# Optimization experiments

Measured on AMD Instinct MI355X. Metric: run time of the kernel, lower is better.

The kernel has to match this reference:

```python
import jax, jax.numpy as jnp
import numpy as np

N_NODES = 50000
N_EDGES = 800000
N_GRAPHS = 512
F_IN = 128
D = 256
EPS = 1e-5
NEG_SLOPE = 0.01  # torch LeakyReLU default


def leaky_relu(x):
    return jnp.where(x >= 0, x, NEG_SLOPE * x)


def egnn_conv(x, edge_index, edge_attr, lin2_w, lin2_b, lin_w, lin_b, n_nodes):
    # message: LeakyReLU(lin(x_j + lin2(edge_attr))), aggregate: add at target i
    src, dst = edge_index[0], edge_index[1]
    ea = edge_attr @ lin2_w.T + lin2_b          # [E, in]
    msg = (x[src] + ea) @ lin_w.T + lin_b        # [E, out]
    msg = leaky_relu(msg)
    return jax.ops.segment_sum(msg, dst, num_segments=n_nodes)


def batch_norm(x, w, b):
    # training-mode BatchNorm1d: biased batch statistics over node axis
    mean = jnp.mean(x, axis=0)
    var = jnp.mean(jnp.square(x - mean), axis=0)
    return (x - mean) * jax.lax.rsqrt(var + EPS) * w + b


def setup_inputs() -> dict:
    key = jax.random.key(0)
    ks = jax.random.split(key, 8)
    inp = {
        "node_ids": jax.random.randint(ks[0], (N_NODES,), 0, 51),
        "edge_index": jax.random.randint(ks[1], (2, N_EDGES), 0, N_NODES),
        "edge_attr": jax.random.normal(ks[2], (N_EDGES, 4), dtype=jnp.float32),
        "batch": jnp.sort(jax.random.randint(ks[3], (N_NODES,), 0, N_GRAPHS)),
        "emb_table": jax.random.normal(ks[4], (51, F_IN), dtype=jnp.float32) * 0.1,
        "c1_lin2_w": jax.random.normal(ks[5], (F_IN, 4), dtype=jnp.float32) * 0.1,
        "c1_lin2_b": jnp.zeros((F_IN,), jnp.float32),
        "c1_lin_w": jax.random.normal(ks[6], (D, F_IN), dtype=jnp.float32) * (1.0 / np.sqrt(F_IN)),
        "c1_lin_b": jnp.zeros((D,), jnp.float32),
        "bn1_w": jnp.ones((D,), jnp.float32),
        "bn1_b": jnp.zeros((D,), jnp.float32),
        "c2_lin2_w": jax.random.normal(jax.random.fold_in(key, 10), (D, 4), dtype=jnp.float32) * 0.1,
        "c2_lin2_b": jnp.zeros((D,), jnp.float32),
        "c2_lin_w": jax.random.normal(ks[7], (D, D), dtype=jnp.float32) * (1.0 / np.sqrt(D)),
        "c2_lin_b": jnp.zeros((D,), jnp.float32),
        "bn2_w": jnp.ones((D,), jnp.float32),
        "bn2_b": jnp.zeros((D,), jnp.float32),
        "gate_w": jax.random.normal(jax.random.fold_in(key, 11), (1, D), dtype=jnp.float32) * 0.1,
        "gate_b": jnp.zeros((1,), jnp.float32),
    }
    return inp


def reference(node_ids, edge_index, edge_attr, batch, emb_table,
              c1_lin2_w, c1_lin2_b, c1_lin_w, c1_lin_b, bn1_w, bn1_b,
              c2_lin2_w, c2_lin2_b, c2_lin_w, c2_lin_b, bn2_w, bn2_b,
              gate_w, gate_b):
    x = emb_table[node_ids]                                   # [N, F_IN]
    x = egnn_conv(x, edge_index, edge_attr, c1_lin2_w, c1_lin2_b,
                  c1_lin_w, c1_lin_b, N_NODES)                # [N, D]
    x = leaky_relu(batch_norm(x, bn1_w, bn1_b))
    x2 = egnn_conv(x, edge_index, edge_attr, c2_lin2_w, c2_lin2_b,
                   c2_lin_w, c2_lin_b, N_NODES)               # [N, D]
    x2 = leaky_relu(batch_norm(x2, bn2_w, bn2_b))
    # AttentionalAggregation: softmax of gate over each graph segment
    gate = x2 @ gate_w.T + gate_b                             # [N, 1]
    gmax = jax.ops.segment_max(gate, batch, num_segments=N_GRAPHS)
    e = jnp.exp(gate - gmax[batch])                           # [N, 1]
    denom = jax.ops.segment_sum(e, batch, num_segments=N_GRAPHS)
    alpha = e / denom[batch]
    out = jax.ops.segment_sum(alpha * x2, batch, num_segments=N_GRAPHS)
    return out                                                # [G, D]
```

## Files before the change

### kernel.cpp

```cpp
#include <hip/hip_runtime.h>
#include <hip/hip_bf16.h>

#define NN 50000
#define NE 800000
#define NG 512

typedef __bf16 bf16_t;
typedef __bf16 bf16x8 __attribute__((ext_vector_type(8)));
typedef __bf16 bf16x4 __attribute__((ext_vector_type(4)));
typedef float f32x4 __attribute__((ext_vector_type(4)));
typedef float f32x2 __attribute__((ext_vector_type(2)));

__device__ __forceinline__ float lrelu(float v) { return v >= 0.f ? v : 0.01f * v; }

__device__ __forceinline__ f32x2 unpk2(unsigned w) {
    union { unsigned u; float f; } lo, hi;
    lo.u = w << 16;
    hi.u = w & 0xffff0000u;
    f32x2 r; r[0] = lo.f; r[1] = hi.f; return r;
}

__device__ __forceinline__ int vzero() {
    int vz;
    asm("v_mov_b32 %0, 0" : "=v"(vz));
    return vz;
}

__global__ void gme_setup(const float* __restrict__ emb,
                          const float* __restrict__ c1lw, const float* __restrict__ c1l2w,
                          const float* __restrict__ c1l2b, const float* __restrict__ c1lb,
                          const float* __restrict__ c2lw, const float* __restrict__ c2l2w,
                          const float* __restrict__ c2l2b, const float* __restrict__ c2lb,
                          bf16_t* __restrict__ TYB, float* __restrict__ WC1,
                          float* __restrict__ WC2, float* __restrict__ CB2,
                          bf16_t* __restrict__ W2B) {
    int b = blockIdx.x, t = threadIdx.x;
    if (b < 51) {
        const float4* er = (const float4*)(emb + b * 128);
        const float4* zb = (const float4*)c1l2b;
        const float4* wr = (const float4*)(c1lw + t * 128);
        float s = 0.f;
        for (int k = 0; k < 32; ++k) {
            float4 e = er[k], z = zb[k], w = wr[k];
            s += (e.x + z.x) * w.x + (e.y + z.y) * w.y + (e.z + z.z) * w.z + (e.w + z.w) * w.w;
        }
        TYB[b * 256 + t] = (bf16_t)(s + c1lb[t]);
    } else if (b == 51) {
        const float4* wr = (const float4*)(c1lw + t * 128);
        const float4* cw = (const float4*)c1l2w;
        float4 a = make_float4(0.f, 0.f, 0.f, 0.f);
        for (int k = 0; k < 32; ++k) {
            float4 w = wr[k];
            float4 c0 = cw[k * 4 + 0], c1 = cw[k * 4 + 1], c2 = cw[k * 4 + 2], c3 = cw[k * 4 + 3];
            a.x += w.x * c0.x + w.y * c1.x + w.z * c2.x + w.w * c3.x;
            a.y += w.x * c0.y + w.y * c1.y + w.z * c2.y + w.w * c3.y;
            a.z += w.x * c0.z + w.y * c1.z + w.z * c2.z + w.w * c3.z;
            a.w += w.x * c0.w + w.y * c1.w + w.z * c2.w + w.w * c3.w;
        }
        ((float4*)WC1)[t] = a;
    } else if (b == 52) {
        const float4* wr = (const float4*)(c2lw + t * 256);
        const float4* cw = (const float4*)c2l2w;
        const float4* zb = (const float4*)c2l2b;
        float4 a = make_float4(0.f, 0.f, 0.f, 0.f);
        float ab = 0.f;
        for (int k = 0; k < 64; ++k) {
            float4 w = wr[k];
            float4 c0 = cw[k * 4 + 0], c1 = cw[k * 4 + 1], c2 = cw[k * 4 + 2], c3 = cw[k * 4 + 3];
            float4 z = zb[k];
            a.x += w.x * c0.x + w.y * c1.x + w.z * c2.x + w.w * c3.x;
            a.y += w.x * c0.y + w.y * c1.y + w.z * c2.y + w.w * c3.y;
            a.z += w.x * c0.z + w.y * c1.z + w.z * c2.z + w.w * c3.z;
            a.w += w.x * c0.w + w.y * c1.w + w.z * c2.w + w.w * c3.w;
            ab += w.x * z.x + w.y * z.y + w.z * z.z + w.w * z.w;
        }
        ((float4*)WC2)[t] = a;
        CB2[t] = ab + c2lb[t];
    } else {
        int i0 = (b - 53) * 1024;
        for (int r = 0; r < 4; ++r) {
            int i = i0 + r * 256 + t;
            W2B[i] = (bf16_t)c2lw[i];
        }
    }
}

__global__ void gme_count(const int* __restrict__ ei, int* __restrict__ cnt) {
    int e = blockIdx.x * 256 + threadIdx.x;
    if (e >= NE) return;
    atomicAdd(&cnt[ei[NE + e]], 1);
}

__global__ void gme_scan1(const int* __restrict__ CNT, int* __restrict__ LP,
                          int* __restrict__ BS) {
    __shared__ int lds[256];
    int b = blockIdx.x, t = threadIdx.x;
    int i = b * 196 + t;
    int v = (t < 196 && i < NN) ? CNT[i] : 0;
    lds[t] = v;
    __syncthreads();
    for (int off = 1; off < 256; off <<= 1) {
        int u = (t >= off) ? lds[t - off] : 0;
        __syncthreads();
        lds[t] += u;
        __syncthreads();
    }
    if (t < 196 && i < NN) LP[i] = lds[t] - v;
    if (t == 255) BS[b] = lds[255];
}

__global__ void gme_scan2(const int* __restrict__ BS, int* __restrict__ BX,
                          int* __restrict__ RS) {
    __shared__ int lds[256];
    int t = threadIdx.x;
    int v = BS[t];
    lds[t] = v;
    __syncthreads();
    for (int off = 1; off < 256; off <<= 1) {
        int u = (t >= off) ? lds[t - off] : 0;
        __syncthreads();
        lds[t] += u;
        __syncthreads();
    }
    BX[t] = lds[t] - v;
    if (t == 255) RS[NN] = lds[255];
}

__global__ void gme_scan3(const int* __restrict__ LP, const int* __restrict__ BX,
                          int* __restrict__ RS, int* __restrict__ CUR) {
    int b = blockIdx.x, t = threadIdx.x;
    if (t >= 196) return;
    int i = b * 196 + t;
    if (i >= NN) return;
    int v = BX[b] + LP[i];
    RS[i] = v;
    CUR[i] = v;
}

__global__ void gme_scatter(const int* __restrict__ ei,
                            const float4* __restrict__ eattr,
                            const int* __restrict__ node_ids,
                            int* __restrict__ CUR, int* __restrict__ SM,
                            float4* __restrict__ SattrP) {
    int e = blockIdx.x * 256 + threadIdx.x;
    if (e >= NE) return;
    int s = ei[e];
    int d = ei[NE + e];
    int nid = node_ids[s];
    int pos = atomicAdd(&CUR[d], 1);
    SM[pos] = s | (nid << 16);
    SattrP[pos] = eattr[e];
}

__global__ __launch_bounds__(256) void gme_conv0(
        const int* __restrict__ RS, const int* __restrict__ SM,
        const float4* __restrict__ SattrP, const bf16_t* __restrict__ TYB,
        const float* __restrict__ Wc, float* __restrict__ agg) {
    __shared__ __align__(16) uint2 sTY[51 * 64];
    {
        const uint4* s4 = (const uint4*)TYB;
        uint4* d4 = (uint4*)sTY;
        for (int i = threadIdx.x; i < 51 * 32; i += 256) d4[i] = s4[i];
    }
    __syncthreads();
    int lane = threadIdx.x & 63;
    int vz = vzero();
    const float4* wc4 = (const float4*)Wc;
    int c4 = lane * 4;
    float4 w0 = wc4[c4 + 0], w1 = wc4[c4 + 1], w2 = wc4[c4 + 2], w3 = wc4[c4 + 3];
    f32x2 wA0 = {w0.x, w1.x}, wB0 = {w0.y, w1.y}, wC0 = {w0.z, w1.z}, wD0 = {w0.w, w1.w};
    f32x2 wA1 = {w2.x, w3.x}, wB1 = {w2.y, w3.y}, wC1 = {w2.z, w3.z}, wD1 = {w2.w, w3.w};
    const f32x2 zero = {0.f, 0.f};
    const uint2* lrow = sTY + lane;
    int base = blockIdx.x * 16 + (threadIdx.x >> 6) * 4;
#pragma unroll 1
    for (int k = 0; k < 4; ++k) {
        int node = __builtin_amdgcn_readfirstlane(base + k);
        int rs = RS[node], re = RS[node + 1];
        f32x2 accP0 = zero, accP1 = zero, accA0 = zero, accA1 = zero;
        auto accum = [&](float4 a, uint2 r) {
            f32x2 y0 = unpk2(r.x), y1 = unpk2(r.y);
            f32x2 ax = {a.x, a.x}, ay = {a.y, a.y}, az = {a.z, a.z}, aw = {a.w, a.w};
            f32x2 m0 = __builtin_elementwise_fma(ax, wA0, y0);
            f32x2 m1 = __builtin_elementwise_fma(ax, wA1, y1);
            m0 = __builtin_elementwise_fma(ay, wB0, m0);
            m1 = __builtin_elementwise_fma(ay, wB1, m1);
            m0 = __builtin_elementwise_fma(az, wC0, m0);
            m1 = __builtin_elementwise_fma(az, wC1, m1);
            m0 = __builtin_elementwise_fma(aw, wD0, m0);
            m1 = __builtin_elementwise_fma(aw, wD1, m1);
            accA0 += m0; accA1 += m1;
            accP0 += __builtin_elementwise_max(m0, zero);
            accP1 += __builtin_elementwise_max(m1, zero);
        };
        int j = rs;
        for (; j + 8 <= re; j += 8) {
            int m[8]; float4 a[8]; uint2 r[8];
#pragma unroll
            for (int u = 0; u < 8; ++u) m[u] = SM[j + u + vz];
#pragma unroll
            for (int u = 0; u < 8; ++u) a[u] = SattrP[j + u + vz];
#pragma unroll
            for (int u = 0; u < 8; ++u) r[u] = lrow[(m[u] >> 16) << 6];
#pragma unroll
            for (int u = 0; u < 8; ++u) accum(a[u], r[u]);
        }
        if (j + 4 <= re) {
            int m[4]; float4 a[4]; uint2 r[4];
#pragma unroll
            for (int u = 0; u < 4; ++u) m[u] = SM[j + u + vz];
#pragma unroll
            for (int u = 0; u < 4; ++u) a[u] = SattrP[j + u + vz];
#pragma unroll
            for (int u = 0; u < 4; ++u) r[u] = lrow[(m[u] >> 16) << 6];
#pragma unroll
            for (int u = 0; u < 4; ++u) accum(a[u], r[u]);
            j += 4;
        }
        for (; j < re; ++j) {
            int m = SM[j + vz];
            accum(SattrP[j + vz], lrow[(m >> 16) << 6]);
        }
        const f32x2 c99 = {0.99f, 0.99f}, c01 = {0.01f, 0.01f};
        f32x2 o0 = __builtin_elementwise_fma(accP0, c99, accA0 * c01);
        f32x2 o1 = __builtin_elementwise_fma(accP1, c99, accA1 * c01);
        *((float4*)(agg + node * 256) + lane) = make_float4(o0[0], o0[1], o1[0], o1[1]);
    }
}

__global__ __launch_bounds__(256, 4) void gme_conv1(
        const int* __restrict__ RS, const int* __restrict__ SM,
        const float4* __restrict__ SattrP, const bf16_t* __restrict__ QB,
        const float* __restrict__ Wc, float* __restrict__ agg) {
    int lane = threadIdx.x & 63;
    int node = __builtin_amdgcn_readfirstlane(blockIdx.x * 4 + (threadIdx.x >> 6));
    if (node >= NN) return;
    const float4* wc4 = (const float4*)Wc;
    int c4 = lane * 4;
    float4 w0 = wc4[c4 + 0], w1 = wc4[c4 + 1], w2 = wc4[c4 + 2], w3 = wc4[c4 + 3];
    f32x2 wA0 = {w0.x, w1.x}, wB0 = {w0.y, w1.y}, wC0 = {w0.z, w1.z}, wD0 = {w0.w, w1.w};
    f32x2 wA1 = {w2.x, w3.x}, wB1 = {w2.y, w3.y}, wC1 = {w2.z, w3.z}, wD1 = {w2.w, w3.w};
    const f32x2 zero = {0.f, 0.f};
    f32x2 accP0 = zero, accP1 = zero, accA0 = zero, accA1 = zero;
    int rs = RS[node], re = RS[node + 1];
    const char* yb = (const char*)QB;
    unsigned loff = (unsigned)(lane << 3);
    auto rowld = [&](int row) -> uint2 {
        return *(const uint2*)(yb + ((unsigned)row << 9) + loff);
    };
    auto accum = [&](float4 a, uint2 r) {
        f32x2 y0 = unpk2(r.x), y1 = unpk2(r.y);
        f32x2 ax = {a.x, a.x}, ay = {a.y, a.y}, az = {a.z, a.z}, aw = {a.w, a.w};
        f32x2 m0 = __builtin_elementwise_fma(ax, wA0, y0);
        f32x2 m1 = __builtin_elementwise_fma(ax, wA1, y1);
        m0 = __builtin_elementwise_fma(ay, wB0, m0);
        m1 = __builtin_elementwise_fma(ay, wB1, m1);
        m0 = __builtin_elementwise_fma(az, wC0, m0);
        m1 = __builtin_elementwise_fma(az, wC1, m1);
        m0 = __builtin_elementwise_fma(aw, wD0, m0);
        m1 = __builtin_elementwise_fma(aw, wD1, m1);
        accA0 += m0; accA1 += m1;
        accP0 += __builtin_elementwise_max(m0, zero);
        accP1 += __builtin_elementwise_max(m1, zero);
    };
    int j = rs;
    for (; j + 12 <= re; j += 12) {
        int s[12]; float4 a[12]; uint2 r[12];
#pragma unroll
        for (int u = 0; u < 12; ++u) s[u] = SM[j + u];
#pragma unroll
        for (int u = 0; u < 12; ++u) r[u] = rowld(s[u] & 0xffff);
#pragma unroll
        for (int u = 0; u < 12; ++u) a[u] = SattrP[j + u];
#pragma unroll
        for (int u = 0; u < 12; ++u) accum(a[u], r[u]);
    }
    if (j + 8 <= re) {
        int s[8]; float4 a[8]; uint2 r[8];
#pragma unroll
        for (int u = 0; u < 8; ++u) s[u] = SM[j + u];
#pragma unroll
        for (int u = 0; u < 8; ++u) r[u] = rowld(s[u] & 0xffff);
#pragma unroll
        for (int u = 0; u < 8; ++u) a[u] = SattrP[j + u];
#pragma unroll
        for (int u = 0; u < 8; ++u) accum(a[u], r[u]);
        j += 8;
    }
    if (j + 4 <= re) {
        int s[4]; float4 a[4]; uint2 r[4];
#pragma unroll
        for (int u = 0; u < 4; ++u) s[u] = SM[j + u];
#pragma unroll
        for (int u = 0; u < 4; ++u) r[u] = rowld(s[u] & 0xffff);
#pragma unroll
        for (int u = 0; u < 4; ++u) a[u] = SattrP[j + u];
#pragma unroll
        for (int u = 0; u < 4; ++u) accum(a[u], r[u]);
        j += 4;
    }
    for (; j < re; ++j) accum(SattrP[j], rowld(SM[j] & 0xffff));
    const f32x2 c99 = {0.99f, 0.99f}, c01 = {0.01f, 0.01f};
    f32x2 o0 = __builtin_elementwise_fma(accP0, c99, accA0 * c01);
    f32x2 o1 = __builtin_elementwise_fma(accP1, c99, accA1 * c01);
    *((float4*)(agg + node * 256) + lane) = make_float4(o0[0], o0[1], o1[0], o1[1]);
}

__global__ __launch_bounds__(256) void gme_bns1(const float* __restrict__ P,
                                                float* __restrict__ PART) {
    __shared__ float ls[4][256], lq[4][256];
    int lane = threadIdx.x & 63;
    int w = threadIdx.x >> 6;
    int b = blockIdx.x;
    int r0 = b * 98;
    int r1 = r0 + 98; if (r1 > NN) r1 = NN;
    float4 s = make_float4(0, 0, 0, 0), q = make_float4(0, 0, 0, 0);
    for (int n = r0 + w; n < r1; n += 4) {
        float4 v = ((const float4*)P)[n * 64 + lane];
        s.x += v.x; s.y += v.y; s.z += v.z; s.w += v.w;
        q.x += v.x * v.x; q.y += v.y * v.y; q.z += v.z * v.z; q.w += v.w * v.w;
    }
    int c = lane * 4;
    ls[w][c] = s.x; ls[w][c + 1] = s.y; ls[w][c + 2] = s.z; ls[w][c + 3] = s.w;
    lq[w][c] = q.x; lq[w][c + 1] = q.y; lq[w][c + 2] = q.z; lq[w][c + 3] = q.w;
    __syncthreads();
    if (w == 0) {
#pragma unroll
        for (int k = 0; k < 4; ++k) {
            int cc = c + k;
            PART[b * 512 + cc] = ls[0][cc] + ls[1][cc] + ls[2][cc] + ls[3][cc];
            PART[b * 512 + 256 + cc] = lq[0][cc] + lq[1][cc] + lq[2][cc] + lq[3][cc];
        }
    }
}

__global__ __launch_bounds__(512) void gme_bns2(const float* __restrict__ PART,
                                                float* __restrict__ ST) {
    int t = threadIdx.x;
    int b = blockIdx.x;
    float acc = 0.f;
#pragma unroll
    for (int r = 0; r < 32; ++r) acc += PART[(b * 32 + r) * 512 + t];
    atomicAdd(&ST[t], acc);
}

__global__ __launch_bounds__(256) void gme_gemm(const float* __restrict__ P,
                                                const float* __restrict__ ST,
                                                const float* __restrict__ bw,
                                                const float* __restrict__ bb,
                                                const bf16_t* __restrict__ W2B,
                                                const float* __restrict__ CB2,
                                                bf16_t* __restrict__ QB) {
    __shared__ float s_sc[256], s_sh[256];
    __shared__ __align__(16) uint4 sB[8192];
    {
        int c = threadIdx.x;
        float mean = ST[c] * (1.f / NN);
        float var = ST[256 + c] * (1.f / NN) - mean * mean;
        float sc = bw[c] * rsqrtf(var + 1e-5f);
        s_sc[c] = sc;
        s_sh[c] = bb[c] - mean * sc;
        const uint4* w4 = (const uint4*)W2B;
#pragma unroll
        for (int it = 0; it < 32; ++it) {
            int i = it * 256 + c;
            int row = i >> 5, slot = i & 31;
            sB[(row << 5) | (slot ^ (row & 7))] = w4[i];
        }
    }
    __syncthreads();
    int lane = threadIdx.x & 63;
    int wave = blockIdx.x * 4 + (threadIdx.x >> 6);
    if (wave >= NN / 16) return;
    int m0 = wave * 16;
    int r = lane & 15, q = lane >> 4;
    int rx = r & 7;
    const float* arow = P + (m0 + r) * 256 + q * 8;
    bf16x8 a[8];
#pragma unroll
    for (int kt = 0; kt < 8; ++kt) {
        int k0 = kt * 32 + q * 8;
        float4 u0 = *(const float4*)(arow + kt * 32);
        float4 u1 = *(const float4*)(arow + kt * 32 + 4);
        bf16x8 f;
        f[0] = (bf16_t)lrelu(fmaf(u0.x, s_sc[k0 + 0], s_sh[k0 + 0]));
        f[1] = (bf16_t)lrelu(fmaf(u0.y, s_sc[k0 + 1], s_sh[k0 + 1]));
        f[2] = (bf16_t)lrelu(fmaf(u0.z, s_sc[k0 + 2], s_sh[k0 + 2]));
        f[3] = (bf16_t)lrelu(fmaf(u0.w, s_sc[k0 + 3], s_sh[k0 + 3]));
        f[4] = (bf16_t)lrelu(fmaf(u1.x, s_sc[k0 + 4], s_sh[k0 + 4]));
        f[5] = (bf16_t)lrelu(fmaf(u1.y, s_sc[k0 + 5], s_sh[k0 + 5]));
        f[6] = (bf16_t)lrelu(fmaf(u1.z, s_sc[k0 + 6], s_sh[k0 + 6]));
        f[7] = (bf16_t)lrelu(fmaf(u1.w, s_sc[k0 + 7], s_sh[k0 + 7]));
        a[kt] = f;
    }
#pragma unroll 1
    for (int g = 0; g < 2; ++g) {
        f32x4 acc[8];
#pragma unroll
        for (int n8 = 0; n8 < 8; ++n8) acc[n8] = (f32x4){0.f, 0.f, 0.f, 0.f};
#pragma unroll
        for (int kt = 0; kt < 8; ++kt) {
            int slot = (kt * 4 + q) ^ rx;
            bf16x8 bf[8];
#pragma unroll
            for (int n8 = 0; n8 < 8; ++n8) {
                int row = g * 128 + n8 * 16 + r;
                bf[n8] = *(const bf16x8*)&sB[(row << 5) | slot];
            }
#pragma unroll
            for (int n8 = 0; n8 < 8; ++n8) {
                acc[n8] = __builtin_amdgcn_mfma_f32_16x16x32_bf16(bf[n8], a[kt], acc[n8], 0, 0, 0);
            }
        }
#pragma unroll
        for (int n8 = 0; n8 < 8; ++n8) {
            int nt = g * 8 + n8;
            float4 cbv = ((const float4*)CB2)[nt * 4 + q];
            bf16x4 o;
            o[0] = (bf16_t)(acc[n8][0] + cbv.x);
            o[1] = (bf16_t)(acc[n8][1] + cbv.y);
            o[2] = (bf16_t)(acc[n8][2] + cbv.z);
            o[3] = (bf16_t)(acc[n8][3] + cbv.w);
            *(bf16x4*)(QB + (m0 + r) * 256 + nt * 16 + q * 4) = o;
        }
    }
}

__global__ void gme_gstart(const int* __restrict__ batch, int* __restrict__ GS) {
    int n = blockIdx.x * 256 + threadIdx.x;
    if (n >= NN) return;
    int b = batch[n];
    if (n == 0) {
        for (int g = 0; g <= b; ++g) GS[g] = 0;
    } else {
        int a = batch[n - 1];
        for (int g = a + 1; g <= b; ++g) GS[g] = n;
    }
    if (n == NN - 1) {
        for (int g = b + 1; g <= NG; ++g) GS[g] = NN;
    }
}

__global__ __launch_bounds__(256) void gme_attn(const int* __restrict__ GS,
                                                const float* __restrict__ P,
                                                const float* __restrict__ ST,
                                                const float* __restrict__ bw,
                                                const float* __restrict__ bb,
                                                const float* __restrict__ gw,
                                                const float* __restrict__ gb,
                                                float* __restrict__ out) {
    __shared__ float gl[1024];
    __shared__ float rr[8];
    int g = blockIdx.x, t = threadIdx.x;
    int lo = GS[g], hi = GS[g + 1];
    if (lo >= hi) { out[g * 256 + t] = 0.f; return; }
    int lane = t & 63, w = t >> 6;
    {
        float4 s4 = ((const float4*)ST)[lane];
        float4 q4 = ((const float4*)(ST + 256))[lane];
        float4 w4 = ((const float4*)bw)[lane];
        float4 b4 = ((const float4*)bb)[lane];
        float4 g4 = ((const float4*)gw)[lane];
        float m0 = s4.x * (1.f / NN), m1 = s4.y * (1.f / NN);
        float m2 = s4.z * (1.f / NN), m3 = s4.w * (1.f / NN);
        float sc0 = w4.x * rsqrtf(q4.x * (1.f / NN) - m0 * m0 + 1e-5f);
        float sc1 = w4.y * rsqrtf(q4.y * (1.f / NN) - m1 * m1 + 1e-5f);
        float sc2 = w4.z * rsqrtf(q4.z * (1.f / NN) - m2 * m2 + 1e-5f);
        float sc3 = w4.w * rsqrtf(q4.w * (1.f / NN) - m3 * m3 + 1e-5f);
        float sh0 = b4.x - m0 * sc0, sh1 = b4.y - m1 * sc1;
        float sh2 = b4.z - m2 * sc2, sh3 = b4.w - m3 * sc3;
        float gb0 = gb[0];
        for (int n = lo + w; n < hi; n += 4) {
            float4 p = *(const float4*)(P + n * 256 + lane * 4);
            float d = lrelu(fmaf(p.x, sc0, sh0)) * g4.x
                    + lrelu(fmaf(p.y, sc1, sh1)) * g4.y
                    + lrelu(fmaf(p.z, sc2, sh2)) * g4.z
                    + lrelu(fmaf(p.w, sc3, sh3)) * g4.w;
#pragma unroll
            for (int off = 32; off > 0; off >>= 1) d += __shfl_xor(d, off, 64);
            if (lane == 0) gl[n - lo] = d + gb0;
        }
    }
    __syncthreads();
    int cnt = hi - lo;
    float lm = -3.0e38f;
    for (int i = t; i < cnt; i += 256) lm = fmaxf(lm, gl[i]);
#pragma unroll
    for (int off = 32; off > 0; off >>= 1) lm = fmaxf(lm, __shfl_xor(lm, off, 64));
    if (lane == 0) rr[w] = lm;
    __syncthreads();
    float mx = fmaxf(fmaxf(rr[0], rr[1]), fmaxf(rr[2], rr[3]));
    float ls = 0.f;
    for (int i = t; i < cnt; i += 256) { float e = expf(gl[i] - mx); gl[i] = e; ls += e; }
#pragma unroll
    for (int off = 32; off > 0; off >>= 1) ls += __shfl_xor(ls, off, 64);
    if (lane == 0) rr[4 + w] = ls;
    __syncthreads();
    float sinv = 1.f / (rr[4] + rr[5] + rr[6] + rr[7]);
    float mean = ST[t] * (1.f / NN);
    float var = ST[256 + t] * (1.f / NN) - mean * mean;
    float sc = bw[t] * rsqrtf(var + 1e-5f);
    float sh = bb[t] - mean * sc;
    float a0 = 0.f, a1 = 0.f, a2 = 0.f, a3 = 0.f;
    int n = lo;
    for (; n + 4 <= hi; n += 4) {
        float p0 = P[n * 256 + t], p1 = P[(n + 1) * 256 + t];
        float p2 = P[(n + 2) * 256 + t], p3 = P[(n + 3) * 256 + t];
        a0 = fmaf(gl[n - lo + 0], lrelu(fmaf(p0, sc, sh)), a0);
        a1 = fmaf(gl[n - lo + 1], lrelu(fmaf(p1, sc, sh)), a1);
        a2 = fmaf(gl[n - lo + 2], lrelu(fmaf(p2, sc, sh)), a2);
        a3 = fmaf(gl[n - lo + 3], lrelu(fmaf(p3, sc, sh)), a3);
    }
    for (; n < hi; ++n) a0 = fmaf(gl[n - lo], lrelu(fmaf(P[n * 256 + t], sc, sh)), a0);
    out[g * 256 + t] = (a0 + a1 + a2 + a3) * sinv;
}

extern "C" void kernel_launch(void* const* d_in, const int* in_sizes, int n_in,
                              void* d_out, int out_size, void* d_ws, size_t ws_size,
                              hipStream_t stream) {
    const int* node_ids = (const int*)d_in[0];
    const int* edge_index = (const int*)d_in[1];
    const float4* edge_attr = (const float4*)d_in[2];
    const int* batch = (const int*)d_in[3];
    const float* emb = (const float*)d_in[4];
    const float* c1l2w = (const float*)d_in[5];
    const float* c1l2b = (const float*)d_in[6];
    const float* c1lw = (const float*)d_in[7];
    const float* c1lb = (const float*)d_in[8];
    const float* bn1w = (const float*)d_in[9];
    const float* bn1b = (const float*)d_in[10];
    const float* c2l2w = (const float*)d_in[11];
    const float* c2l2b = (const float*)d_in[12];
    const float* c2lw = (const float*)d_in[13];
    const float* c2lb = (const float*)d_in[14];
    const float* bn2w = (const float*)d_in[15];
    const float* bn2b = (const float*)d_in[16];
    const float* gate_w = (const float*)d_in[17];
    const float* gate_b = (const float*)d_in[18];

    char* ws = (char*)d_ws;
    size_t oP = 0;
    size_t oQB = oP + 51200000;
    size_t oSattrP = oQB + 25600000;
    size_t oSM = oSattrP + 12800000;
    size_t oRS = oSM + 3200000;
    size_t oCNT = oRS + 200064;
    size_t oCUR = oCNT + 200000;
    size_t oLP = oCUR + 200000;
    size_t oBS = oLP + 200000;
    size_t oBX = oBS + 1024;
    size_t oTY = oBX + 1024;
    size_t oWC1 = oTY + 52224;
    size_t oWC2 = oWC1 + 4096;
    size_t oCB2 = oWC2 + 4096;
    size_t oW2B = oCB2 + 1024;
    size_t oST = oW2B + 131072;
    size_t oGS = oST + 4096;
    size_t oPART = oGS + 2064;

    float* P = (float*)(ws + oP);
    bf16_t* QB = (bf16_t*)(ws + oQB);
    float4* SattrP = (float4*)(ws + oSattrP);
    int* SM = (int*)(ws + oSM);
    int* RS = (int*)(ws + oRS);
    int* CNT = (int*)(ws + oCNT);
    int* CUR = (int*)(ws + oCUR);
    int* LP = (int*)(ws + oLP);
    int* BS = (int*)(ws + oBS);
    int* BX = (int*)(ws + oBX);
    bf16_t* TYB = (bf16_t*)(ws + oTY);
    float* WC1 = (float*)(ws + oWC1);
    float* WC2 = (float*)(ws + oWC2);
    float* CB2 = (float*)(ws + oCB2);
    bf16_t* W2B = (bf16_t*)(ws + oW2B);
    float* ST1 = (float*)(ws + oST);
    float* ST2 = ST1 + 512;
    int* GS = (int*)(ws + oGS);
    float* PART = (float*)(ws + oPART);

    hipMemsetAsync(CNT, 0, NN * sizeof(int), stream);
    hipMemsetAsync(ST1, 0, 4096, stream);

    gme_setup<<<117, 256, 0, stream>>>(emb, c1lw, c1l2w, c1l2b, c1lb,
                                       c2lw, c2l2w, c2l2b, c2lb,
                                       TYB, WC1, WC2, CB2, W2B);
    gme_count<<<NE / 256, 256, 0, stream>>>(edge_index, CNT);
    gme_scan1<<<256, 256, 0, stream>>>(CNT, LP, BS);
    gme_scan2<<<1, 256, 0, stream>>>(BS, BX, RS);
    gme_scan3<<<256, 256, 0, stream>>>(LP, BX, RS, CUR);
    gme_scatter<<<NE / 256, 256, 0, stream>>>(edge_index, edge_attr, node_ids,
                                              CUR, SM, SattrP);
    gme_gstart<<<(NN + 255) / 256, 256, 0, stream>>>(batch, GS);
    gme_conv0<<<NN / 16, 256, 0, stream>>>(RS, SM, SattrP, TYB, WC1, P);
    gme_bns1<<<512, 256, 0, stream>>>(P, PART);
    gme_bns2<<<16, 512, 0, stream>>>(PART, ST1);
    gme_gemm<<<(NN / 16 + 3) / 4, 256, 0, stream>>>(P, ST1, bn1w, bn1b, W2B, CB2, QB);
    gme_conv1<<<NN / 4, 256, 0, stream>>>(RS, SM, SattrP, QB, WC2, P);
    gme_bns1<<<512, 256, 0, stream>>>(P, PART);
    gme_bns2<<<16, 512, 0, stream>>>(PART, ST2);
    gme_attn<<<NG, 256, 0, stream>>>(GS, P, ST2, bn2w, bn2b, gate_w, gate_b,
                                     (float*)d_out);
}
```

Measured before the change: 409.6 us.

## Fuse first BatchNorm statistics into conv0 and deepen its edge-loop unroll

```diff
diff --git a/kernel.cpp b/kernel.cpp
--- a/kernel.cpp
+++ b/kernel.cpp
@@ -152,10 +152,11 @@
     SattrP[pos] = eattr[e];
 }
 
-__global__ __launch_bounds__(256) void gme_conv0(
+__global__ __launch_bounds__(256, 4) void gme_conv0(
         const int* __restrict__ RS, const int* __restrict__ SM,
         const float4* __restrict__ SattrP, const bf16_t* __restrict__ TYB,
-        const float* __restrict__ Wc, float* __restrict__ agg) {
+        const float* __restrict__ Wc, float* __restrict__ agg,
+        float* __restrict__ PART) {
     __shared__ __align__(16) uint2 sTY[51 * 64];
     {
         const uint4* s4 = (const uint4*)TYB;
@@ -164,6 +165,7 @@
     }
     __syncthreads();
     int lane = threadIdx.x & 63;
+    int w = threadIdx.x >> 6;
     int vz = vzero();
     const float4* wc4 = (const float4*)Wc;
     int c4 = lane * 4;
@@ -172,7 +174,8 @@
     f32x2 wA1 = {w2.x, w3.x}, wB1 = {w2.y, w3.y}, wC1 = {w2.z, w3.z}, wD1 = {w2.w, w3.w};
     const f32x2 zero = {0.f, 0.f};
     const uint2* lrow = sTY + lane;
-    int base = blockIdx.x * 16 + (threadIdx.x >> 6) * 4;
+    int base = blockIdx.x * 16 + w * 4;
+    f32x2 ssum0 = zero, ssum1 = zero, qsum0 = zero, qsum1 = zero;
 #pragma unroll 1
     for (int k = 0; k < 4; ++k) {
         int node = __builtin_amdgcn_readfirstlane(base + k);
@@ -194,25 +197,47 @@
             accP1 += __builtin_elementwise_max(m1, zero);
         };
         int j = rs;
-        for (; j + 8 <= re; j += 8) {
+        for (; j + 16 <= re; j += 16) {
+            int m[16]; uint2 r[16];
+#pragma unroll
+            for (int u = 0; u < 16; ++u) m[u] = SM[j + u + vz];
+#pragma unroll
+            for (int u = 0; u < 16; ++u) r[u] = lrow[(m[u] >> 16) << 6];
+            {
+                float4 a[8];
+#pragma unroll
+                for (int u = 0; u < 8; ++u) a[u] = SattrP[j + u + vz];
+#pragma unroll
+                for (int u = 0; u < 8; ++u) accum(a[u], r[u]);
+            }
+            {
+                float4 a[8];
+#pragma unroll
+                for (int u = 0; u < 8; ++u) a[u] = SattrP[j + 8 + u + vz];
+#pragma unroll
+                for (int u = 0; u < 8; ++u) accum(a[u], r[8 + u]);
+            }
+        }
+        if (j + 8 <= re) {
             int m[8]; float4 a[8]; uint2 r[8];
 #pragma unroll
             for (int u = 0; u < 8; ++u) m[u] = SM[j + u + vz];
 #pragma unroll
+            for (int u = 0; u < 8; ++u) r[u] = lrow[(m[u] >> 16) << 6];
+#pragma unroll
             for (int u = 0; u < 8; ++u) a[u] = SattrP[j + u + vz];
 #pragma unroll
-            for (int u = 0; u < 8; ++u) r[u] = lrow[(m[u] >> 16) << 6];
-#pragma unroll
             for (int u = 0; u < 8; ++u) accum(a[u], r[u]);
+            j += 8;
         }
         if (j + 4 <= re) {
             int m[4]; float4 a[4]; uint2 r[4];
 #pragma unroll
             for (int u = 0; u < 4; ++u) m[u] = SM[j + u + vz];
 #pragma unroll
+            for (int u = 0; u < 4; ++u) r[u] = lrow[(m[u] >> 16) << 6];
+#pragma unroll
             for (int u = 0; u < 4; ++u) a[u] = SattrP[j + u + vz];
-#pragma unroll
-            for (int u = 0; u < 4; ++u) r[u] = lrow[(m[u] >> 16) << 6];
 #pragma unroll
             for (int u = 0; u < 4; ++u) accum(a[u], r[u]);
             j += 4;
@@ -225,7 +250,21 @@
         f32x2 o0 = __builtin_elementwise_fma(accP0, c99, accA0 * c01);
         f32x2 o1 = __builtin_elementwise_fma(accP1, c99, accA1 * c01);
         *((float4*)(agg + node * 256) + lane) = make_float4(o0[0], o0[1], o1[0], o1[1]);
-    }
+        ssum0 += o0; ssum1 += o1;
+        qsum0 += o0 * o0; qsum1 += o1 * o1;
+    }
+    __syncthreads();
+    float* red = (float*)sTY;
+    red[w * 512 + c4 + 0] = ssum0[0]; red[w * 512 + c4 + 1] = ssum0[1];
+    red[w * 512 + c4 + 2] = ssum1[0]; red[w * 512 + c4 + 3] = ssum1[1];
+    red[w * 512 + 256 + c4 + 0] = qsum0[0]; red[w * 512 + 256 + c4 + 1] = qsum0[1];
+    red[w * 512 + 256 + c4 + 2] = qsum1[0]; red[w * 512 + 256 + c4 + 3] = qsum1[1];
+    __syncthreads();
+    int cc = threadIdx.x;
+    float s = red[cc] + red[512 + cc] + red[1024 + cc] + red[1536 + cc];
+    float q = red[256 + cc] + red[768 + cc] + red[1280 + cc] + red[1792 + cc];
+    PART[blockIdx.x * 512 + cc] = s;
+    PART[blockIdx.x * 512 + 256 + cc] = q;
 }
 
 __global__ __launch_bounds__(256, 4) void gme_conv1(
@@ -344,6 +383,17 @@
     atomicAdd(&ST[t], acc);
 }
 
+__global__ __launch_bounds__(512) void gme_bns2b(const float* __restrict__ PART,
+                                                 float* __restrict__ ST) {
+    int t = threadIdx.x;
+    int b = blockIdx.x;
+    int r0 = b * 32;
+    int r1 = r0 + 32; if (r1 > 3125) r1 = 3125;
+    float acc = 0.f;
+    for (int r = r0; r < r1; ++r) acc += PART[r * 512 + t];
+    atomicAdd(&ST[t], acc);
+}
+
 __global__ __launch_bounds__(256) void gme_gemm(const float* __restrict__ P,
                                                 const float* __restrict__ ST,
                                                 const float* __restrict__ bw,
@@ -591,9 +641,8 @@
     gme_scatter<<<NE / 256, 256, 0, stream>>>(edge_index, edge_attr, node_ids,
                                               CUR, SM, SattrP);
     gme_gstart<<<(NN + 255) / 256, 256, 0, stream>>>(batch, GS);
-    gme_conv0<<<NN / 16, 256, 0, stream>>>(RS, SM, SattrP, TYB, WC1, P);
-    gme_bns1<<<512, 256, 0, stream>>>(P, PART);
-    gme_bns2<<<16, 512, 0, stream>>>(PART, ST1);
+    gme_conv0<<<NN / 16, 256, 0, stream>>>(RS, SM, SattrP, TYB, WC1, P, PART);
+    gme_bns2b<<<98, 512, 0, stream>>>(PART, ST1);
     gme_gemm<<<(NN / 16 + 3) / 4, 256, 0, stream>>>(P, ST1, bn1w, bn1b, W2B, CB2, QB);
     gme_conv1<<<NN / 4, 256, 0, stream>>>(RS, SM, SattrP, QB, WC2, P);
     gme_bns1<<<512, 256, 0, stream>>>(P, PART);
```

Result: slower. 431.9 us (+5.4%).
